# Performance work log

Hardware: AMD Instinct MI355X
Metric: run time of the kernel (lower is better)

## Reference

```python
import jax, jax.numpy as jnp
import numpy as np

D_MODEL = 1024
NUM_HEADS = 16
D_K = D_MODEL // NUM_HEADS
B, S = 4, 2048
NEG_INF = -1e9


def _linear_params(key, d_out, d_in):
    k1, k2 = jax.random.split(key)
    lim = 1.0 / np.sqrt(d_in)
    w = jax.random.uniform(k1, (d_out, d_in), jnp.float32, -lim, lim)
    b = jax.random.uniform(k2, (d_out,), jnp.float32, -lim, lim)
    return w, b


def setup_inputs() -> dict:
    key = jax.random.key(0)
    ks = jax.random.split(key, 16)
    query = jax.random.normal(ks[0], (B, S, D_MODEL), jnp.float32)
    kk = jax.random.normal(ks[1], (B, S, D_MODEL), jnp.float32)
    vv = jax.random.normal(ks[2], (B, S, D_MODEL), jnp.float32)
    # causal mask, broadcastable to [B,H,Sq,Sk]
    mask = jnp.tril(jnp.ones((S, S), jnp.int32))[None, None]
    wq1, bq1 = _linear_params(ks[3], D_MODEL, D_MODEL)
    wq2, bq2 = _linear_params(ks[4], D_MODEL, D_MODEL)
    wk1, bk1 = _linear_params(ks[5], D_MODEL, D_MODEL)
    wk2, bk2 = _linear_params(ks[6], D_MODEL, D_MODEL)
    wv1, bv1 = _linear_params(ks[7], D_MODEL, D_MODEL)
    wv2, bv2 = _linear_params(ks[8], D_MODEL, D_MODEL)
    wo, bo = _linear_params(ks[9], D_MODEL, D_MODEL)
    return dict(query=query, key=kk, value=vv, mask=mask,
                wq1=wq1, bq1=bq1, wq2=wq2, bq2=bq2,
                wk1=wk1, bk1=bk1, wk2=wk2, bk2=bk2,
                wv1=wv1, bv1=bv1, wv2=wv2, bv2=bv2,
                wo=wo, bo=bo)


def _swiglu_proj(x, w1, b1, w2, b2):
    # F.silu(w1(x)) * w2(x)
    return jax.nn.silu(x @ w1.T + b1) * (x @ w2.T + b2)


def _split_heads(x):
    b, s, _ = x.shape
    return x.reshape(b, s, NUM_HEADS, D_K).transpose(0, 2, 1, 3)  # [B,H,S,dk]


def reference(query, key, value, mask,
              wq1, bq1, wq2, bq2,
              wk1, bk1, wk2, bk2,
              wv1, bv1, wv2, bv2,
              wo, bo):
    q = _split_heads(_swiglu_proj(query, wq1, bq1, wq2, bq2))
    k = _split_heads(_swiglu_proj(key, wk1, bk1, wk2, bk2))
    v = _split_heads(_swiglu_proj(value, wv1, bv1, wv2, bv2))
    scores = jnp.einsum('bhqd,bhkd->bhqk', q, k) / np.sqrt(D_K).astype(np.float32)
    scores = jnp.where(mask == 0, jnp.float32(NEG_INF), scores)
    attn = jax.nn.softmax(scores, axis=-1)
    x = jnp.einsum('bhqk,bhkd->bhqd', attn, v)  # [B,H,S,dk]
    x = x.transpose(0, 2, 1, 3).reshape(query.shape[0], -1, NUM_HEADS * D_K)
    return x @ wo.T + bo
```

## Files before the change

### kernel.cpp

```cpp
#include <hip/hip_runtime.h>


typedef __bf16 bf16;
typedef bf16 bf16x8 __attribute__((ext_vector_type(8)));
typedef float f32x4 __attribute__((ext_vector_type(4)));
typedef unsigned short u16;
typedef unsigned int u32;
typedef u16 u16x8 __attribute__((ext_vector_type(8)));
typedef u16 u16x4 __attribute__((ext_vector_type(4)));

#define DEVI static __device__ __forceinline__

DEVI u16 f2b(float f) {
  union { float f; u32 u; } v; v.f = f;
  u32 r = v.u + 0x7FFFu + ((v.u >> 16) & 1u);
  return (u16)(r >> 16);
}
DEVI f32x4 mfma16(bf16x8 a, bf16x8 b, f32x4 c) {
  return __builtin_amdgcn_mfma_f32_16x16x32_bf16(a, b, c, 0, 0, 0);
}
DEVI void gload16(const void* g, void* l) {
  __builtin_amdgcn_global_load_lds(
      (const __attribute__((address_space(1))) void*)g,
      (__attribute__((address_space(3))) void*)l, 16, 0, 0);
}
DEVI u32 cvtpk(float lo, float hi) {
  u32 r;
  asm("v_cvt_pk_bf16_f32 %0, %1, %2" : "=v"(r) : "v"(lo), "v"(hi));
  return r;
}
DEVI void pswap(u32& a, u32& b) {
  asm("v_permlane32_swap_b32 %0, %1" : "+v"(a), "+v"(b));
}

struct P6 { const float* p[6]; };

__global__ void cvt_wpair(P6 in, u16* __restrict__ out) {
  const int pair = blockIdx.y;
  const float* w1 = in.p[2 * pair];
  const float* w2 = in.p[2 * pair + 1];
  u16* dst = out + (size_t)pair * 2097152;
  const int i = blockIdx.x * 256 + threadIdx.x;
  const int v = i >> 7;
  const int k0 = (i & 127) << 3;
  const int t7 = v & 127;
  const int g = (t7 >> 4) & 1;
  const int c = (v >> 7) * 64 + ((t7 >> 5) << 4) + (t7 & 15);
  const float* src = (g ? w2 : w1) + (size_t)c * 1024 + k0;
  const f32x4 a = *(const f32x4*)src;
  const f32x4 b = *(const f32x4*)(src + 4);
  u16x8 wv;
#pragma unroll
  for (int j = 0; j < 4; ++j) { wv[j] = f2b(a[j]); wv[4 + j] = f2b(b[j]); }
  *(u16x8*)(dst + (size_t)v * 1024 + k0) = wv;
}

__global__ void cvt_x(const float* __restrict__ s0, u16* __restrict__ d0,
                      const float* __restrict__ s1, u16* __restrict__ d1) {
  const float* src = blockIdx.y ? s1 : s0;
  u16* dst = blockIdx.y ? d1 : d0;
  const int i = blockIdx.x * 256 + threadIdx.x;
  const f32x4 a = ((const f32x4*)src)[i * 2];
  const f32x4 b = ((const f32x4*)src)[i * 2 + 1];
  u16x8 w;
#pragma unroll
  for (int j = 0; j < 4; ++j) { w[j] = f2b(a[j]); w[4 + j] = f2b(b[j]); }
  ((u16x8*)dst)[i] = w;
}

struct GArgs {
  const u16* A; const u16* W;
  const float* b1; const float* b2;
  void* out; float scale;
};

template<int MODE, bool DUAL>
__global__ __launch_bounds__(512, 2) void gemm256(GArgs g0, GArgs g1)
{
  extern __shared__ char smem[];
  const int fl = blockIdx.x;
  const GArgs g = (DUAL && fl >= 512) ? g1 : g0;
  const int local = DUAL ? (fl & 511) : fl;
  const int t = threadIdx.x;
  const int lane = t & 63, wid = t >> 6;
  const int lg = lane >> 4, lc = lane & 15;
  const int wr = (wid >> 1) * 64;
  const int wc = (wid & 1) * 64;
  constexpr int NXB = (MODE == 2) ? 8 : 16;
  const int xcd = local & 7, w8 = local >> 3;
  const int m0 = (xcd * 4 + w8 / NXB) * 256;
  const int bx = w8 % NXB;
  const int K = 1024;
  const int srow = lane >> 3, scolb = (lane & 7) << 4;

  const f32x4 fz = {0.f, 0.f, 0.f, 0.f};
  f32x4 acc[4][4];
#pragma unroll
  for (int i = 0; i < 4; ++i)
#pragma unroll
    for (int j = 0; j < 4; ++j) acc[i][j] = fz;

  auto STAGE = [&](int buf, int kt) {
    const int k0 = kt << 6;
    char* As = smem + buf * 49152;
    char* Ws = As + 32768;
#pragma unroll
    for (int p = 0; p < 4; ++p) {
      const int rb = wid * 32 + p * 8;
      const int row = rb + srow;
      const int ce = (scolb ^ ((row & 7) << 4)) >> 1;
      gload16(g.A + (size_t)(m0 + row) * K + k0 + ce, As + rb * 128);
    }
#pragma unroll
    for (int p = 0; p < 2; ++p) {
      const int rb = wid * 16 + p * 8;
      const int row = rb + srow;
      const int ce = (scolb ^ ((row & 7) << 4)) >> 1;
      gload16(g.W + (size_t)(bx * 128 + row) * K + k0 + ce, Ws + rb * 128);
    }
  };

  STAGE(0, 0);
  __syncthreads();
  for (int kt = 0; kt < 16; ++kt) {
    const int cur = kt & 1;
    if (kt < 15) STAGE(cur ^ 1, kt + 1);
    const char* As = smem + cur * 49152;
    const char* Ws = As + 32768;
#pragma unroll
    for (int kh = 0; kh < 2; ++kh) {
      bf16x8 af[4], bfr[4];
#pragma unroll
      for (int mf = 0; mf < 4; ++mf) {
        const int r = wr + mf * 16 + lc;
        af[mf] = *(const bf16x8*)(As + r * 128 + ((kh * 64 + (lg << 4)) ^ ((r & 7) << 4)));
      }
#pragma unroll
      for (int nf = 0; nf < 4; ++nf) {
        const int v = wc + nf * 16 + lc;
        bfr[nf] = *(const bf16x8*)(Ws + v * 128 + ((kh * 64 + (lg << 4)) ^ ((v & 7) << 4)));
      }
#pragma unroll
      for (int mf = 0; mf < 4; ++mf)
#pragma unroll
        for (int nf = 0; nf < 4; ++nf)
          acc[mf][nf] = mfma16(af[mf], bfr[nf], acc[mf][nf]);
    }
    __syncthreads();
  }
  if constexpr (MODE == 2) {
    float* Co = (float*)g.out;
#pragma unroll
    for (int mf = 0; mf < 4; ++mf)
#pragma unroll
      for (int nf = 0; nf < 4; ++nf) {
        const int r0 = m0 + wr + mf * 16 + (lg << 2);
        const int C = bx * 128 + wc + nf * 16 + lc;
        const float bv = g.b1[C];
#pragma unroll
        for (int j = 0; j < 4; ++j)
          Co[(size_t)(r0 + j) * 1024 + C] = acc[mf][nf][j] + bv;
      }
  } else {
    u16* Co = (u16*)g.out;
#pragma unroll
    for (int mf = 0; mf < 4; ++mf) {
      const int r0 = m0 + wr + mf * 16 + (lg << 2);
#pragma unroll
      for (int p = 0; p < 2; ++p) {
        const int C = bx * 64 + (wid & 1) * 32 + p * 16 + lc;
        const float b1v = g.b1[C], b2v = g.b2[C];
        const int h = C >> 6, d = C & 63;
        if constexpr (MODE == 0) {
#pragma unroll
          for (int j = 0; j < 4; ++j) {
            const int r = r0 + j;
            const float x = acc[mf][2 * p][j] + b1v;
            const float y = acc[mf][2 * p + 1][j] + b2v;
            const float vv = (x / (1.f + __expf(-x))) * y * g.scale;
            const int bb = r >> 11, s = r & 2047;
            Co[((size_t)(bb * 16 + h) * 2048 + s) * 64 + d] = f2b(vv);
          }
        } else {
          u16x4 wv;
#pragma unroll
          for (int j = 0; j < 4; ++j) {
            const float x = acc[mf][2 * p][j] + b1v;
            const float y = acc[mf][2 * p + 1][j] + b2v;
            wv[j] = f2b((x / (1.f + __expf(-x))) * y);
          }
          const int bb = r0 >> 11, s0 = r0 & 2047;
          *(u16x4*)(Co + ((size_t)(bb * 16 + h) * 64 + d) * 2048 + s0) = wv;
        }
      }
    }
  }
}

__global__ __launch_bounds__(64, 2) void attn_fwd(
    const u16* __restrict__ Q, const u16* __restrict__ Kk,
    const u16* __restrict__ Vt, u16* __restrict__ O)
{
  const int lane = threadIdx.x;
  const int lg = lane >> 4, lc = lane & 15;
  const int flat = blockIdx.y * 32 + blockIdx.x;
  const int fl2 = (flat & 7) * 256 + (flat >> 3);
  const int qi = fl2 & 31;
  const int bh = fl2 >> 5;
  const int b = bh >> 4, h = bh & 15;
  const f32x4 fz = {0.f, 0.f, 0.f, 0.f};
  const float THR = 11.5f;
  const bool ev = ((lg & 1) == 0);

  const u16* Kb = Kk + (size_t)bh * 2048 * 64;
  const u16* Vb = Vt + (size_t)bh * 64 * 2048;

  for (int pass = 0; pass < 2; ++pass) {
    const int qc = pass ? (63 - qi) : qi;
    const int qw = qc * 32;
    const int nt = (qc >> 1) + 1;

    bf16x8 qf[2][2];
#pragma unroll
    for (int qg = 0; qg < 2; ++qg)
#pragma unroll
      for (int kh = 0; kh < 2; ++kh)
        qf[qg][kh] = *(const bf16x8*)(Q + ((size_t)bh * 2048 + qw + qg * 16 + lc) * 64 + kh * 32 + lg * 8);

    f32x4 o[2][4];
#pragma unroll
    for (int qg = 0; qg < 2; ++qg)
#pragma unroll
      for (int dn = 0; dn < 4; ++dn) o[qg][dn] = fz;
    float mrow[2] = {-1e30f, -1e30f}, lsum[2] = {0.f, 0.f};

    bf16x8 kra[8], krb[8], vr[8];

    auto LOADK = [&](bf16x8 (&kr)[8], int kt) {
      const int kbase = kt << 6;
#pragma unroll
      for (int nf = 0; nf < 4; ++nf)
#pragma unroll
        for (int kh = 0; kh < 2; ++kh)
          kr[nf * 2 + kh] = *(const bf16x8*)(Kb + (size_t)(kbase + nf * 16 + lc) * 64 + kh * 32 + lg * 8);
    };

    auto BODY = [&](bf16x8 (&kr)[8], int kt) {
      const int kbase = kt << 6;
#pragma unroll
      for (int dn = 0; dn < 4; ++dn)
#pragma unroll
        for (int kh = 0; kh < 2; ++kh)
          vr[dn * 2 + kh] = *(const bf16x8*)(Vb + (size_t)(dn * 16 + lc) * 2048 + kbase + kh * 32 + lg * 8);
      f32x4 sfT[4][2];
#pragma unroll
      for (int nf = 0; nf < 4; ++nf)
#pragma unroll
        for (int qg = 0; qg < 2; ++qg) sfT[nf][qg] = fz;
      __builtin_amdgcn_s_setprio(1);
#pragma unroll
      for (int kh = 0; kh < 2; ++kh)
#pragma unroll
        for (int nf = 0; nf < 4; ++nf) {
          sfT[nf][0] = mfma16(kr[nf * 2 + kh], qf[0][kh], sfT[nf][0]);
          sfT[nf][1] = mfma16(kr[nf * 2 + kh], qf[1][kh], sfT[nf][1]);
        }
      __builtin_amdgcn_s_setprio(0);
      if (kt == nt - 1) {
#pragma unroll
        for (int qg = 0; qg < 2; ++qg) {
          const int qq = qw + qg * 16 + lc;
#pragma unroll
          for (int nf = 0; nf < 4; ++nf)
#pragma unroll
            for (int j = 0; j < 4; ++j)
              if (kbase + nf * 16 + (lg << 2) + j > qq) sfT[nf][qg][j] = -1e30f;
        }
      }
      float pm[2];
#pragma unroll
      for (int qg = 0; qg < 2; ++qg) {
        float m = sfT[0][qg][0];
#pragma unroll
        for (int nf = 0; nf < 4; ++nf)
#pragma unroll
          for (int j = 0; j < 4; ++j) m = fmaxf(m, sfT[nf][qg][j]);
        m = fmaxf(m, __shfl_xor(m, 16));
        m = fmaxf(m, __shfl_xor(m, 32));
        pm[qg] = m;
      }
      const bool ok = (pm[0] <= mrow[0] + THR) && (pm[1] <= mrow[1] + THR);
      if (!__all(ok)) {
#pragma unroll
        for (int qg = 0; qg < 2; ++qg) {
          const float mn = fmaxf(mrow[qg], pm[qg]);
          const float sc = exp2f(mrow[qg] - mn);
          mrow[qg] = mn;
          lsum[qg] *= sc;
#pragma unroll
          for (int dn = 0; dn < 4; ++dn)
#pragma unroll
            for (int j = 0; j < 4; ++j) o[qg][dn][j] *= sc;
        }
      }
#pragma unroll
      for (int qg = 0; qg < 2; ++qg)
#pragma unroll
        for (int nf = 0; nf < 4; ++nf)
#pragma unroll
          for (int j = 0; j < 4; ++j) {
            const float p = exp2f(sfT[nf][qg][j] - mrow[qg]);
            sfT[nf][qg][j] = p;
            lsum[qg] += p;
          }
      u32 pw[2][2][4];
#pragma unroll
      for (int qg = 0; qg < 2; ++qg)
#pragma unroll
        for (int kh = 0; kh < 2; ++kh) {
          u32 A0 = cvtpk(sfT[2 * kh][qg][0], sfT[2 * kh][qg][1]);
          u32 A1 = cvtpk(sfT[2 * kh][qg][2], sfT[2 * kh][qg][3]);
          u32 B0 = cvtpk(sfT[2 * kh + 1][qg][0], sfT[2 * kh + 1][qg][1]);
          u32 B1 = cvtpk(sfT[2 * kh + 1][qg][2], sfT[2 * kh + 1][qg][3]);
          pswap(A0, B0);
          pswap(A1, B1);
          const u32 P0s = __shfl_xor(A0, 16);
          const u32 Q0s = __shfl_xor(B0, 16);
          const u32 P1s = __shfl_xor(A1, 16);
          const u32 Q1s = __shfl_xor(B1, 16);
          pw[qg][kh][0] = ev ? A0 : Q0s;
          pw[qg][kh][1] = ev ? A1 : Q1s;
          pw[qg][kh][2] = ev ? P0s : B0;
          pw[qg][kh][3] = ev ? P1s : B1;
        }
      __builtin_amdgcn_s_setprio(1);
#pragma unroll
      for (int kh = 0; kh < 2; ++kh) {
        union { u32 u[4]; bf16x8 v; } p0, p1;
#pragma unroll
        for (int w = 0; w < 4; ++w) { p0.u[w] = pw[0][kh][w]; p1.u[w] = pw[1][kh][w]; }
#pragma unroll
        for (int dn = 0; dn < 4; ++dn) {
          o[0][dn] = mfma16(vr[dn * 2 + kh], p0.v, o[0][dn]);
          o[1][dn] = mfma16(vr[dn * 2 + kh], p1.v, o[1][dn]);
        }
      }
      __builtin_amdgcn_s_setprio(0);
    };

    LOADK(kra, 0);
    for (int kt = 0; kt < nt; kt += 2) {
      if (kt + 1 < nt) LOADK(krb, kt + 1);
      BODY(kra, kt);
      if (kt + 2 < nt) LOADK(kra, kt + 2);
      if (kt + 1 < nt) BODY(krb, kt + 1);
    }
#pragma unroll
    for (int qg = 0; qg < 2; ++qg) {
      float l = lsum[qg];
      l += __shfl_xor(l, 16);
      l += __shfl_xor(l, 32);
      const float inv = __builtin_amdgcn_rcpf(l);
      const size_t ob = ((size_t)(b * 2048 + qw + qg * 16 + lc) * 16 + h) * 64 + (lg << 2);
#pragma unroll
      for (int dn = 0; dn < 4; ++dn) {
        u16x4 wv;
#pragma unroll
        for (int j = 0; j < 4; ++j) wv[j] = f2b(o[qg][dn][j] * inv);
        *(u16x4*)(O + ob + dn * 16) = wv;
      }
    }
  }
}

extern "C" void kernel_launch(void* const* d_in, const int* in_sizes, int n_in,
                              void* d_out, int out_size, void* d_ws, size_t ws_size,
                              hipStream_t stream)
{
  (void)in_sizes; (void)n_in; (void)out_size; (void)ws_size;
  const float* xq  = (const float*)d_in[0];
  const float* xk  = (const float*)d_in[1];
  const float* xv  = (const float*)d_in[2];
  const float* wq1 = (const float*)d_in[4];
  const float* bq1 = (const float*)d_in[5];
  const float* wq2 = (const float*)d_in[6];
  const float* bq2 = (const float*)d_in[7];
  const float* wk1 = (const float*)d_in[8];
  const float* bk1 = (const float*)d_in[9];
  const float* wk2 = (const float*)d_in[10];
  const float* bk2 = (const float*)d_in[11];
  const float* wv1 = (const float*)d_in[12];
  const float* bv1 = (const float*)d_in[13];
  const float* wv2 = (const float*)d_in[14];
  const float* bv2 = (const float*)d_in[15];
  const float* wo  = (const float*)d_in[16];
  const float* bo  = (const float*)d_in[17];

  char* ws = (char*)d_ws;
  u16* WB = (u16*)ws;
  u16* XQ = (u16*)(ws + 14680064);
  u16* XK = (u16*)(ws + 31457280);
  u16* QB = (u16*)(ws + 48234496);
  u16* KB = (u16*)(ws + 65011712);
  u16* VT = (u16*)(ws + 81788928);
  u16* XV = XQ;
  u16* AO = XK;
  u16* WCQ = WB;
  u16* WCK = WB + 2097152;
  u16* WCV = WB + 4194304;
  u16* WO  = WB + 6291456;

  P6 p6 = {{wq1, wq2, wk1, wk2, wv1, wv2}};
  cvt_wpair<<<dim3(1024, 3), 256, 0, stream>>>(p6, WB);
  cvt_x<<<dim3(512, 1), 256, 0, stream>>>(wo, WO, wo, WO);
  cvt_x<<<dim3(4096, 2), 256, 0, stream>>>(xq, XQ, xk, XK);

  const float QSCALE = 0.125f * 1.44269504088896f;
  GArgs gq = {XQ, WCQ, bq1, bq2, QB, QSCALE};
  GArgs gk = {XK, WCK, bk1, bk2, KB, 1.0f};
  gemm256<0, true><<<1024, 512, 98304, stream>>>(gq, gk);

  cvt_x<<<dim3(4096, 1), 256, 0, stream>>>(xv, XV, xv, XV);
  GArgs gv = {XV, WCV, bv1, bv2, VT, 1.0f};
  gemm256<1, false><<<512, 512, 98304, stream>>>(gv, gv);

  attn_fwd<<<dim3(32, 64), 64, 0, stream>>>(QB, KB, VT, AO);

  GArgs go = {AO, WO, bo, nullptr, d_out, 1.0f};
  gemm256<2, false><<<256, 512, 98304, stream>>>(go, go);
}
```

Measured before the change: 290.4 us.

## Share K/V tiles across four attention waves via double-buffered LDS

Attention moves from one-wave blocks, where each wave loaded K and V straight from global memory into registers, to 4-wave blocks covering 128 query rows. The block stages each 64-key K and V tile into swizzled, double-buffered shared memory with async global-to-LDS loads, and all four waves read from it. This cuts redundant global K/V traffic by sharing tiles across waves. In exchange it adds block-wide barriers every key tile, and waves whose rows are fully masked sit idle inside the causal diagonal tiles.

Measured after the change: 251.8 us. 1.15x faster.

```diff
diff --git a/kernel.cpp b/kernel.cpp
--- a/kernel.cpp
+++ b/kernel.cpp
@@ -197,28 +197,43 @@
   }
 }
 
-__global__ __launch_bounds__(64, 2) void attn_fwd(
+__global__ __launch_bounds__(256, 2) void attn_fwd(
     const u16* __restrict__ Q, const u16* __restrict__ Kk,
     const u16* __restrict__ Vt, u16* __restrict__ O)
 {
-  const int lane = threadIdx.x;
+  __shared__ char smem[32768];
+  const int t = threadIdx.x;
+  const int lane = t & 63, wid = t >> 6;
   const int lg = lane >> 4, lc = lane & 15;
-  const int flat = blockIdx.y * 32 + blockIdx.x;
-  const int fl2 = (flat & 7) * 256 + (flat >> 3);
-  const int qi = fl2 & 31;
-  const int bh = fl2 >> 5;
+  const int flat = blockIdx.y * 8 + blockIdx.x;
+  const int fl2 = (flat & 7) * 64 + (flat >> 3);
+  const int ci = fl2 & 7;
+  const int bh = fl2 >> 3;
   const int b = bh >> 4, h = bh & 15;
   const f32x4 fz = {0.f, 0.f, 0.f, 0.f};
   const float THR = 11.5f;
   const bool ev = ((lg & 1) == 0);
 
-  const u16* Kb = Kk + (size_t)bh * 2048 * 64;
-  const u16* Vb = Vt + (size_t)bh * 64 * 2048;
+  auto STAGE = [&](int buf, int kt) {
+    const int kbase = kt << 6;
+    char* Kb = smem + buf * 16384;
+    char* Vb = Kb + 8192;
+#pragma unroll
+    for (int p = 0; p < 4; ++p) {
+      const int idx = wid * 4 + p;
+      const int rb = (idx & 7) * 8;
+      const int row = rb + (lane >> 3);
+      const int ce = (((lane & 7) << 4) ^ ((row & 7) << 4)) >> 1;
+      if (idx < 8)
+        gload16(Kk + ((size_t)bh * 2048 + kbase + row) * 64 + ce, Kb + rb * 128);
+      else
+        gload16(Vt + ((size_t)bh * 64 + row) * 2048 + kbase + ce, Vb + rb * 128);
+    }
+  };
 
   for (int pass = 0; pass < 2; ++pass) {
-    const int qc = pass ? (63 - qi) : qi;
-    const int qw = qc * 32;
-    const int nt = (qc >> 1) + 1;
+    const int qc = pass ? (15 - ci) : ci;
+    const int qw = qc * 128 + wid * 32;
 
     bf16x8 qf[2][2];
 #pragma unroll
@@ -234,126 +249,121 @@
       for (int dn = 0; dn < 4; ++dn) o[qg][dn] = fz;
     float mrow[2] = {-1e30f, -1e30f}, lsum[2] = {0.f, 0.f};
 
-    bf16x8 kra[8], krb[8], vr[8];
-
-    auto LOADK = [&](bf16x8 (&kr)[8], int kt) {
+    const int nt = 2 * qc + 2;
+    STAGE(0, 0);
+    __syncthreads();
+    for (int kt = 0; kt < nt; ++kt) {
+      const int cur = kt & 1;
+      if (kt + 1 < nt) STAGE(cur ^ 1, kt + 1);
       const int kbase = kt << 6;
-#pragma unroll
-      for (int nf = 0; nf < 4; ++nf)
-#pragma unroll
-        for (int kh = 0; kh < 2; ++kh)
-          kr[nf * 2 + kh] = *(const bf16x8*)(Kb + (size_t)(kbase + nf * 16 + lc) * 64 + kh * 32 + lg * 8);
-    };
-
-    auto BODY = [&](bf16x8 (&kr)[8], int kt) {
-      const int kbase = kt << 6;
-#pragma unroll
-      for (int dn = 0; dn < 4; ++dn)
-#pragma unroll
-        for (int kh = 0; kh < 2; ++kh)
-          vr[dn * 2 + kh] = *(const bf16x8*)(Vb + (size_t)(dn * 16 + lc) * 2048 + kbase + kh * 32 + lg * 8);
-      f32x4 sfT[4][2];
-#pragma unroll
-      for (int nf = 0; nf < 4; ++nf)
-#pragma unroll
-        for (int qg = 0; qg < 2; ++qg) sfT[nf][qg] = fz;
-      __builtin_amdgcn_s_setprio(1);
-#pragma unroll
-      for (int kh = 0; kh < 2; ++kh)
-#pragma unroll
-        for (int nf = 0; nf < 4; ++nf) {
-          sfT[nf][0] = mfma16(kr[nf * 2 + kh], qf[0][kh], sfT[nf][0]);
-          sfT[nf][1] = mfma16(kr[nf * 2 + kh], qf[1][kh], sfT[nf][1]);
-        }
-      __builtin_amdgcn_s_setprio(0);
-      if (kt == nt - 1) {
+      const char* Ks = smem + cur * 16384;
+      const char* Vs = Ks + 8192;
+      if (kbase <= qw + 31) {
+        f32x4 sfT[4][2];
+#pragma unroll
+        for (int nf = 0; nf < 4; ++nf)
+#pragma unroll
+          for (int qg = 0; qg < 2; ++qg) sfT[nf][qg] = fz;
+        __builtin_amdgcn_s_setprio(1);
+#pragma unroll
+        for (int kh = 0; kh < 2; ++kh) {
+          bf16x8 kb[4];
+#pragma unroll
+          for (int nf = 0; nf < 4; ++nf) {
+            const int r = nf * 16 + lc;
+            kb[nf] = *(const bf16x8*)(Ks + r * 128 + ((kh * 64 + (lg << 4)) ^ ((r & 7) << 4)));
+          }
+#pragma unroll
+          for (int nf = 0; nf < 4; ++nf) {
+            sfT[nf][0] = mfma16(kb[nf], qf[0][kh], sfT[nf][0]);
+            sfT[nf][1] = mfma16(kb[nf], qf[1][kh], sfT[nf][1]);
+          }
+        }
+        __builtin_amdgcn_s_setprio(0);
+        if (kbase + 63 > qw) {
+#pragma unroll
+          for (int qg = 0; qg < 2; ++qg) {
+            const int qq = qw + qg * 16 + lc;
+#pragma unroll
+            for (int nf = 0; nf < 4; ++nf)
+#pragma unroll
+              for (int j = 0; j < 4; ++j)
+                if (kbase + nf * 16 + (lg << 2) + j > qq) sfT[nf][qg][j] = -1e30f;
+          }
+        }
+        float pm[2];
 #pragma unroll
         for (int qg = 0; qg < 2; ++qg) {
-          const int qq = qw + qg * 16 + lc;
+          float m = sfT[0][qg][0];
 #pragma unroll
           for (int nf = 0; nf < 4; ++nf)
 #pragma unroll
-            for (int j = 0; j < 4; ++j)
-              if (kbase + nf * 16 + (lg << 2) + j > qq) sfT[nf][qg][j] = -1e30f;
-        }
-      }
-      float pm[2];
-#pragma unroll
-      for (int qg = 0; qg < 2; ++qg) {
-        float m = sfT[0][qg][0];
-#pragma unroll
-        for (int nf = 0; nf < 4; ++nf)
-#pragma unroll
-          for (int j = 0; j < 4; ++j) m = fmaxf(m, sfT[nf][qg][j]);
-        m = fmaxf(m, __shfl_xor(m, 16));
-        m = fmaxf(m, __shfl_xor(m, 32));
-        pm[qg] = m;
-      }
-      const bool ok = (pm[0] <= mrow[0] + THR) && (pm[1] <= mrow[1] + THR);
-      if (!__all(ok)) {
-#pragma unroll
-        for (int qg = 0; qg < 2; ++qg) {
-          const float mn = fmaxf(mrow[qg], pm[qg]);
-          const float sc = exp2f(mrow[qg] - mn);
-          mrow[qg] = mn;
-          lsum[qg] *= sc;
-#pragma unroll
-          for (int dn = 0; dn < 4; ++dn)
-#pragma unroll
-            for (int j = 0; j < 4; ++j) o[qg][dn][j] *= sc;
-        }
-      }
-#pragma unroll
-      for (int qg = 0; qg < 2; ++qg)
-#pragma unroll
-        for (int nf = 0; nf < 4; ++nf)
-#pragma unroll
-          for (int j = 0; j < 4; ++j) {
-            const float p = exp2f(sfT[nf][qg][j] - mrow[qg]);
-            sfT[nf][qg][j] = p;
-            lsum[qg] += p;
-          }
-      u32 pw[2][2][4];
-#pragma unroll
-      for (int qg = 0; qg < 2; ++qg)
+            for (int j = 0; j < 4; ++j) m = fmaxf(m, sfT[nf][qg][j]);
+          m = fmaxf(m, __shfl_xor(m, 16));
+          m = fmaxf(m, __shfl_xor(m, 32));
+          pm[qg] = m;
+        }
+        const bool ok = (pm[0] <= mrow[0] + THR) && (pm[1] <= mrow[1] + THR);
+        if (!__all(ok)) {
+#pragma unroll
+          for (int qg = 0; qg < 2; ++qg) {
+            const float mn = fmaxf(mrow[qg], pm[qg]);
+            const float sc = exp2f(mrow[qg] - mn);
+            mrow[qg] = mn;
+            lsum[qg] *= sc;
+#pragma unroll
+            for (int dn = 0; dn < 4; ++dn)
+#pragma unroll
+              for (int j = 0; j < 4; ++j) o[qg][dn][j] *= sc;
+          }
+        }
+#pragma unroll
+        for (int qg = 0; qg < 2; ++qg)
+#pragma unroll
+          for (int nf = 0; nf < 4; ++nf)
+#pragma unroll
+            for (int j = 0; j < 4; ++j) {
+              const float p = exp2f(sfT[nf][qg][j] - mrow[qg]);
+              sfT[nf][qg][j] = p;
+              lsum[qg] += p;
+            }
+        u32 pw[2][2][4];
+#pragma unroll
+        for (int qg = 0; qg < 2; ++qg)
+#pragma unroll
+          for (int kh = 0; kh < 2; ++kh) {
+            u32 A0 = cvtpk(sfT[2 * kh][qg][0], sfT[2 * kh][qg][1]);
+            u32 A1 = cvtpk(sfT[2 * kh][qg][2], sfT[2 * kh][qg][3]);
+            u32 B0 = cvtpk(sfT[2 * kh + 1][qg][0], sfT[2 * kh + 1][qg][1]);
+            u32 B1 = cvtpk(sfT[2 * kh + 1][qg][2], sfT[2 * kh + 1][qg][3]);
+            pswap(A0, B0);
+            pswap(A1, B1);
+            const u32 P0s = __shfl_xor(A0, 16);
+            const u32 Q0s = __shfl_xor(B0, 16);
+            const u32 P1s = __shfl_xor(A1, 16);
+            const u32 Q1s = __shfl_xor(B1, 16);
+            pw[qg][kh][0] = ev ? A0 : Q0s;
+            pw[qg][kh][1] = ev ? A1 : Q1s;
+            pw[qg][kh][2] = ev ? P0s : B0;
+            pw[qg][kh][3] = ev ? P1s : B1;
+          }
+        __builtin_amdgcn_s_setprio(1);
 #pragma unroll
         for (int kh = 0; kh < 2; ++kh) {
-          u32 A0 = cvtpk(sfT[2 * kh][qg][0], sfT[2 * kh][qg][1]);
-          u32 A1 = cvtpk(sfT[2 * kh][qg][2], sfT[2 * kh][qg][3]);
-          u32 B0 = cvtpk(sfT[2 * kh + 1][qg][0], sfT[2 * kh + 1][qg][1]);
-          u32 B1 = cvtpk(sfT[2 * kh + 1][qg][2], sfT[2 * kh + 1][qg][3]);
-          pswap(A0, B0);
-          pswap(A1, B1);
-          const u32 P0s = __shfl_xor(A0, 16);
-          const u32 Q0s = __shfl_xor(B0, 16);
-          const u32 P1s = __shfl_xor(A1, 16);
-          const u32 Q1s = __shfl_xor(B1, 16);
-          pw[qg][kh][0] = ev ? A0 : Q0s;
-          pw[qg][kh][1] = ev ? A1 : Q1s;
-          pw[qg][kh][2] = ev ? P0s : B0;
-          pw[qg][kh][3] = ev ? P1s : B1;
-        }
-      __builtin_amdgcn_s_setprio(1);
-#pragma unroll
-      for (int kh = 0; kh < 2; ++kh) {
-        union { u32 u[4]; bf16x8 v; } p0, p1;
-#pragma unroll
-        for (int w = 0; w < 4; ++w) { p0.u[w] = pw[0][kh][w]; p1.u[w] = pw[1][kh][w]; }
-#pragma unroll
-        for (int dn = 0; dn < 4; ++dn) {
-          o[0][dn] = mfma16(vr[dn * 2 + kh], p0.v, o[0][dn]);
-          o[1][dn] = mfma16(vr[dn * 2 + kh], p1.v, o[1][dn]);
-        }
-      }
-      __builtin_amdgcn_s_setprio(0);
-    };
-
-    LOADK(kra, 0);
-    for (int kt = 0; kt < nt; kt += 2) {
-      if (kt + 1 < nt) LOADK(krb, kt + 1);
-      BODY(kra, kt);
-      if (kt + 2 < nt) LOADK(kra, kt + 2);
-      if (kt + 1 < nt) BODY(krb, kt + 1);
+          union { u32 u[4]; bf16x8 v; } p0, p1;
+#pragma unroll
+          for (int w = 0; w < 4; ++w) { p0.u[w] = pw[0][kh][w]; p1.u[w] = pw[1][kh][w]; }
+#pragma unroll
+          for (int dn = 0; dn < 4; ++dn) {
+            const int vr = dn * 16 + lc;
+            const bf16x8 vb = *(const bf16x8*)(Vs + vr * 128 + ((kh * 64 + (lg << 4)) ^ ((vr & 7) << 4)));
+            o[0][dn] = mfma16(vb, p0.v, o[0][dn]);
+            o[1][dn] = mfma16(vb, p1.v, o[1][dn]);
+          }
+        }
+        __builtin_amdgcn_s_setprio(0);
+      }
+      __syncthreads();
     }
 #pragma unroll
     for (int qg = 0; qg < 2; ++qg) {
@@ -424,7 +434,7 @@
   GArgs gv = {XV, WCV, bv1, bv2, VT, 1.0f};
   gemm256<1, false><<<512, 512, 98304, stream>>>(gv, gv);
 
-  attn_fwd<<<dim3(32, 64), 64, 0, stream>>>(QB, KB, VT, AO);
+  attn_fwd<<<dim3(8, 64), 256, 0, stream>>>(QB, KB, VT, AO);
 
   GArgs go = {AO, WO, bo, nullptr, d_out, 1.0f};
   gemm256<2, false><<<256, 512, 98304, stream>>>(go, go);
```
